# Kernel optimization log

Measured on AMD Instinct MI355X. Metric: run time of the kernel, lower is better.

The kernel has to match this reference:

```python
import jax, jax.numpy as jnp
import numpy as np

B, C, H, W, HEADS = 8, 256, 64, 64, 4
EPS = 1e-5  # torch InstanceNorm2d default eps


def conv1x1(x, w):
    # w: [out_c, in_c]; x: [b, in_c, h, w]
    return jnp.einsum('oc,bchw->bohw', w, x)


def maxpool2(x):
    b, c, h, w = x.shape
    return x.reshape(b, c, h // 2, 2, w // 2, 2).max(axis=(3, 5))


def inorm_affine(x, g, b):
    # InstanceNorm2d(affine=True): normalize per (batch, channel) over H,W
    m = jnp.mean(x, axis=(2, 3), keepdims=True)
    v = jnp.mean((x - m) ** 2, axis=(2, 3), keepdims=True)
    return (x - m) * jax.lax.rsqrt(v + EPS) * g[None, :, None, None] + b[None, :, None, None]


def setup_inputs() -> dict:
    key = jax.random.key(0)
    ks = jax.random.split(key, 12)
    s = 1.0 / np.sqrt(C)  # fan-in style scaling for 1x1 conv weights
    return {
        'x': jax.random.normal(ks[0], (B, C, H, W), jnp.float32),
        'theta_w': jax.random.normal(ks[1], (C, C), jnp.float32) * s,
        'phi_w': jax.random.normal(ks[2], (C, C), jnp.float32) * s,
        'g_w': jax.random.normal(ks[3], (C // 2, C), jnp.float32) * s,
        'o_w': jax.random.normal(ks[4], (C, C // 2), jnp.float32) * np.sqrt(2.0 / C),
        'nt_w': 1.0 + 0.1 * jax.random.normal(ks[5], (C,), jnp.float32),
        'nt_b': 0.1 * jax.random.normal(ks[6], (C,), jnp.float32),
        'np_w': 1.0 + 0.1 * jax.random.normal(ks[7], (C,), jnp.float32),
        'np_b': 0.1 * jax.random.normal(ks[8], (C,), jnp.float32),
        'ng_w': 1.0 + 0.1 * jax.random.normal(ks[9], (C // 2,), jnp.float32),
        'ng_b': 0.1 * jax.random.normal(ks[10], (C // 2,), jnp.float32),
        'gamma': jnp.float32(0.5),
    }


def reference(x, theta_w, phi_w, g_w, o_w, nt_w, nt_b, np_w, np_b, ng_w, ng_b, gamma):
    b, c, h, w = x.shape
    n = h * w            # query length
    m = n // 4           # key/value length after 2x2 maxpool
    theta = inorm_affine(conv1x1(x, theta_w), nt_w, nt_b)
    phi = inorm_affine(maxpool2(conv1x1(x, phi_w)), np_w, np_b)
    g = inorm_affine(maxpool2(conv1x1(x, g_w)), ng_w, ng_b)
    # custom head layout: channel dim split as (C//heads, heads), head dim INNER
    theta_ = theta.reshape(b, c // HEADS, HEADS, n)
    phi_ = phi.reshape(b, c // HEADS, HEADS, m)
    g_ = g.reshape(b, (c // 2) // HEADS, HEADS, m)
    beta = jax.nn.softmax(jnp.einsum('bchi,bchj->bhij', theta_, phi_), axis=-1)
    o = jnp.einsum('bchj,bhij->bchi', g_, beta).reshape(b, c // 2, h, w)
    o = conv1x1(o, o_w)
    return gamma * o + x
```

## Files before the change

### kernel.cpp

```cpp
#include <hip/hip_runtime.h>
#include <hip/hip_bf16.h>
#include <math.h>

typedef float f32x4 __attribute__((ext_vector_type(4)));
typedef float f32x16 __attribute__((ext_vector_type(16)));
typedef __bf16 b16x8 __attribute__((ext_vector_type(8)));
typedef __bf16 b16x4 __attribute__((ext_vector_type(4)));
typedef unsigned int u32x2 __attribute__((ext_vector_type(2)));
typedef unsigned int u32x4 __attribute__((ext_vector_type(4)));

#define L2E 1.44269504088896340736f

__global__ void prep_weights(const float* tw, const float* pw, const float* gw,
                             const float* ow, __bf16* Wp, __bf16* OWp) {
    int idx = blockIdx.x * 256 + threadIdx.x;
    if (idx < 640 * 256) {
        int m = idx >> 8, k = idx & 255;
        float v;
        if (m < 256)      { int o = ((m & 63) << 2) + (m >> 6);            v = tw[o * 256 + k]; }
        else if (m < 512) { int mm = m - 256; int o = ((mm & 63) << 2) + (mm >> 6); v = pw[o * 256 + k]; }
        else              { int mm = m - 512; int o = ((mm & 31) << 2) + (mm >> 5); v = gw[o * 256 + k]; }
        Wp[idx] = (__bf16)v;
    } else {
        int j = idx - 640 * 256;
        if (j < 256 * 128) {
            int m = j >> 7, c = j & 127;
            int o = ((c & 31) << 2) + (c >> 5);
            OWp[j] = (__bf16)ow[m * 128 + o];
        }
    }
}

__global__ __launch_bounds__(256) void conv_gemm(const __bf16* __restrict__ Wp,
                                                 const float* __restrict__ x,
                                                 __bf16* theta_t, __bf16* phi_t, __bf16* g_t) {
    int b = blockIdx.z, mt = blockIdx.y, nt = blockIdx.x;
    __shared__ __bf16 Al[128 * 40];
    __shared__ __bf16 Bl[128 * 40];
    int tid = threadIdx.x, l = tid & 63, w = tid >> 6;
    int wm = w >> 1, wn = w & 1, lr = l & 15, lg = l >> 4;
    f32x4 acc[4][4];
#pragma unroll
    for (int i = 0; i < 4; i++)
#pragma unroll
        for (int j = 0; j < 4; j++)
#pragma unroll
            for (int r = 0; r < 4; r++) acc[i][j][r] = 0.f;
    const __bf16* Ag = Wp + (size_t)mt * 128 * 256;
    const float* Bx = x + (size_t)b * 1048576 + nt * 128;
    int srow = tid >> 2, scol = (tid & 3) * 8;
    int bn = tid & 127, bk0 = (tid >> 7) * 8;
    b16x8 aR[2];
    float xr[2][8];
#pragma unroll
    for (int hh = 0; hh < 2; hh++)
        aR[hh] = *(const b16x8*)&Ag[(size_t)(srow + hh * 64) * 256 + scol];
#pragma unroll
    for (int u = 0; u < 2; u++)
#pragma unroll
        for (int e = 0; e < 8; e++)
            xr[u][e] = Bx[(size_t)(bk0 + u * 16 + e) * 4096 + bn];
    for (int k0 = 0; k0 < 256; k0 += 32) {
        if (k0) __syncthreads();
#pragma unroll
        for (int hh = 0; hh < 2; hh++)
            *(b16x8*)&Al[(srow + hh * 64) * 40 + scol] = aR[hh];
#pragma unroll
        for (int u = 0; u < 2; u++) {
            b16x8 v;
#pragma unroll
            for (int e = 0; e < 8; e++) v[e] = (__bf16)xr[u][e];
            *(b16x8*)&Bl[bn * 40 + bk0 + u * 16] = v;
        }
        __syncthreads();
        if (k0 < 224) {
#pragma unroll
            for (int hh = 0; hh < 2; hh++)
                aR[hh] = *(const b16x8*)&Ag[(size_t)(srow + hh * 64) * 256 + k0 + 32 + scol];
#pragma unroll
            for (int u = 0; u < 2; u++)
#pragma unroll
                for (int e = 0; e < 8; e++)
                    xr[u][e] = Bx[(size_t)(k0 + 32 + bk0 + u * 16 + e) * 4096 + bn];
        }
        int ko = lg * 8;
        b16x8 af[4], bfr[4];
#pragma unroll
        for (int i = 0; i < 4; i++) af[i]  = *(b16x8*)&Al[(wm * 64 + i * 16 + lr) * 40 + ko];
#pragma unroll
        for (int i = 0; i < 4; i++) bfr[i] = *(b16x8*)&Bl[(wn * 64 + i * 16 + lr) * 40 + ko];
#pragma unroll
        for (int i = 0; i < 4; i++)
#pragma unroll
            for (int j = 0; j < 4; j++)
                acc[i][j] = __builtin_amdgcn_mfma_f32_16x16x32_bf16(af[i], bfr[j], acc[i][j], 0, 0, 0);
    }
    int rbase = lg * 4;
#pragma unroll
    for (int i = 0; i < 4; i++) {
        int m = mt * 128 + wm * 64 + i * 16 + rbase;
#pragma unroll
        for (int j = 0; j < 4; j++) {
            int p = nt * 128 + wn * 64 + j * 16 + lr;
            b16x4 v;
#pragma unroll
            for (int r = 0; r < 4; r++) v[r] = (__bf16)acc[i][j][r];
            if (m < 256)      *(b16x4*)&theta_t[((size_t)b * 4096 + p) * 256 + m] = v;
            else if (m < 512) *(b16x4*)&phi_t[((size_t)b * 4096 + p) * 256 + (m - 256)] = v;
            else              *(b16x4*)&g_t[((size_t)b * 4096 + p) * 128 + (m - 512)] = v;
        }
    }
}

__global__ __launch_bounds__(256) void theta_stats(const __bf16* __restrict__ src,
                                                   float* p1, float* p2) {
    __shared__ float S1[8][256], S2[8][256];
    int b = blockIdx.y, blk = blockIdx.x;
    int tid = threadIdx.x, cg = tid & 31, rg = tid >> 5;
    float a1[8], a2[8];
#pragma unroll
    for (int e = 0; e < 8; e++) { a1[e] = 0.f; a2[e] = 0.f; }
    const __bf16* base = src + ((size_t)b * 4096 + blk * 64 + rg * 8) * 256 + cg * 8;
#pragma unroll
    for (int r = 0; r < 8; r++) {
        b16x8 v = *(const b16x8*)&base[(size_t)r * 256];
#pragma unroll
        for (int e = 0; e < 8; e++) { float f = (float)v[e]; a1[e] += f; a2[e] += f * f; }
    }
#pragma unroll
    for (int e = 0; e < 8; e++) { S1[rg][cg * 8 + e] = a1[e]; S2[rg][cg * 8 + e] = a2[e]; }
    __syncthreads();
    float s1 = 0.f, s2 = 0.f;
#pragma unroll
    for (int i = 0; i < 8; i++) { s1 += S1[i][tid]; s2 += S2[i][tid]; }
    p1[(b * 64 + blk) * 256 + tid] = s1;
    p2[(b * 64 + blk) * 256 + tid] = s2;
}

__global__ __launch_bounds__(256) void pool_phi(const __bf16* __restrict__ src, __bf16* dst,
                                                float* p1, float* p2) {
    __shared__ float S1[8][256], S2[8][256];
    int b = blockIdx.y, qc = blockIdx.x;
    int tid = threadIdx.x, cg = tid & 31, qg = tid >> 5;
    float a1[8], a2[8];
#pragma unroll
    for (int e = 0; e < 8; e++) { a1[e] = 0.f; a2[e] = 0.f; }
#pragma unroll
    for (int qq = 0; qq < 4; qq++) {
        int q = qc * 32 + qg * 4 + qq, qy = q >> 5, qx = q & 31;
        size_t base = ((size_t)(b * 4096) + qy * 128 + qx * 2) * 256 + cg * 8;
        b16x8 v0 = *(const b16x8*)&src[base];
        b16x8 v1 = *(const b16x8*)&src[base + 256];
        b16x8 v2 = *(const b16x8*)&src[base + 16384];
        b16x8 v3 = *(const b16x8*)&src[base + 16640];
        b16x8 mv;
#pragma unroll
        for (int e = 0; e < 8; e++) {
            float m = fmaxf(fmaxf((float)v0[e], (float)v1[e]), fmaxf((float)v2[e], (float)v3[e]));
            mv[e] = (__bf16)m; a1[e] += m; a2[e] += m * m;
        }
        *(b16x8*)&dst[((size_t)b * 1024 + q) * 256 + cg * 8] = mv;
    }
#pragma unroll
    for (int e = 0; e < 8; e++) { S1[qg][cg * 8 + e] = a1[e]; S2[qg][cg * 8 + e] = a2[e]; }
    __syncthreads();
    float s1 = 0.f, s2 = 0.f;
#pragma unroll
    for (int i = 0; i < 8; i++) { s1 += S1[i][tid]; s2 += S2[i][tid]; }
    p1[(b * 32 + qc) * 256 + tid] = s1;
    p2[(b * 32 + qc) * 256 + tid] = s2;
}

__global__ __launch_bounds__(256) void pool_gT(const __bf16* __restrict__ src, __bf16* gT,
                                               float* p1, float* p2) {
    __shared__ __bf16 Pt[64][136];
    __shared__ float S1[16][128], S2[16][128];
    int b = blockIdx.y, qc = blockIdx.x;
    int tid = threadIdx.x, cg = tid & 15, qg = tid >> 4;
    float a1[8], a2[8];
#pragma unroll
    for (int e = 0; e < 8; e++) { a1[e] = 0.f; a2[e] = 0.f; }
#pragma unroll
    for (int qq = 0; qq < 4; qq++) {
        int ql = qg * 4 + qq, q = qc * 64 + ql;
        int qy = q >> 5, qx = q & 31;
        size_t base = ((size_t)(b * 4096) + qy * 128 + qx * 2) * 128 + cg * 8;
        b16x8 v0 = *(const b16x8*)&src[base];
        b16x8 v1 = *(const b16x8*)&src[base + 128];
        b16x8 v2 = *(const b16x8*)&src[base + 8192];
        b16x8 v3 = *(const b16x8*)&src[base + 8320];
        b16x8 mv;
#pragma unroll
        for (int e = 0; e < 8; e++) {
            float m = fmaxf(fmaxf((float)v0[e], (float)v1[e]), fmaxf((float)v2[e], (float)v3[e]));
            mv[e] = (__bf16)m; a1[e] += m; a2[e] += m * m;
        }
        *(b16x8*)&Pt[ql][cg * 8] = mv;
    }
#pragma unroll
    for (int e = 0; e < 8; e++) { S1[qg][cg * 8 + e] = a1[e]; S2[qg][cg * 8 + e] = a2[e]; }
    __syncthreads();
    if (tid < 128) {
        float s1 = 0.f, s2 = 0.f;
#pragma unroll
        for (int i = 0; i < 16; i++) { s1 += S1[i][tid]; s2 += S2[i][tid]; }
        p1[(b * 16 + qc) * 128 + tid] = s1;
        p2[(b * 16 + qc) * 128 + tid] = s2;
    }
    int c = tid & 127, qh = tid >> 7;
    int hh = c >> 5, ch = c & 31;
#pragma unroll
    for (int sg = 0; sg < 4; sg++) {
        int seg = qh * 4 + sg;
        b16x8 v;
#pragma unroll
        for (int e = 0; e < 8; e++) v[e] = Pt[seg * 8 + e][c];
        *(b16x8*)&gT[((((size_t)(b * 4 + hh) * 16 + qc) * 8 + seg) * 32 + ch) * 8] = v;
    }
}

__global__ void finalize_stats(const float* tp1, const float* tp2, const float* pp1,
                               const float* pp2, const float* gp1, const float* gp2,
                               const float* ntw, const float* ntb, const float* npw,
                               const float* npb, const float* ngw, const float* ngb,
                               float* sct, float* bit, float* scp, float* bip,
                               float* scg, float* big) {
    int idx = blockIdx.x * 256 + threadIdx.x;
    if (idx >= 8 * 640) return;
    int b = idx / 640, c = idx % 640;
    if (c < 256) {
        float s1 = 0.f, s2 = 0.f;
        for (int i = 0; i < 64; i++) { s1 += tp1[(b * 64 + i) * 256 + c]; s2 += tp2[(b * 64 + i) * 256 + c]; }
        float n = 4096.f;
        float m = s1 / n, v = s2 / n - m * m;
        float r = rsqrtf(v + 1e-5f);
        int o = ((c & 63) << 2) + (c >> 6);
        float wv = ntw[o], bv = ntb[o];
        sct[b * 256 + c] = r * wv * L2E;
        bit[b * 256 + c] = (bv - m * r * wv) * L2E;
    } else if (c < 512) {
        int cc = c - 256;
        float s1 = 0.f, s2 = 0.f;
        for (int i = 0; i < 32; i++) { s1 += pp1[(b * 32 + i) * 256 + cc]; s2 += pp2[(b * 32 + i) * 256 + cc]; }
        float n = 1024.f;
        float m = s1 / n, v = s2 / n - m * m;
        float r = rsqrtf(v + 1e-5f);
        int o = ((cc & 63) << 2) + (cc >> 6);
        float wv = npw[o], bv = npb[o];
        scp[b * 256 + cc] = r * wv; bip[b * 256 + cc] = bv - m * r * wv;
    } else {
        int cc = c - 512;
        float s1 = 0.f, s2 = 0.f;
        for (int i = 0; i < 16; i++) { s1 += gp1[(b * 16 + i) * 128 + cc]; s2 += gp2[(b * 16 + i) * 128 + cc]; }
        float n = 1024.f;
        float m = s1 / n, v = s2 / n - m * m;
        float r = rsqrtf(v + 1e-5f);
        int o = ((cc & 31) << 2) + (cc >> 5);
        float wv = ngw[o], bv = ngb[o];
        scg[b * 128 + cc] = r * wv; big[b * 128 + cc] = bv - m * r * wv;
    }
}

__global__ void normalize_phi(const __bf16* __restrict__ php, __bf16* __restrict__ phk,
                              const float* __restrict__ scp, const float* __restrict__ bip) {
    int blk = blockIdx.x, t = threadIdx.x;
    int b = blk >> 6, h = (blk >> 4) & 3, cc = blk & 15;
#pragma unroll
    for (int uu = 0; uu < 2; uu++) {
        int u = uu * 256 + t;
        int slot = u >> 6, key = u & 63;
        int q = cc * 64 + key;
        int cfull = h * 64 + (slot >> 1) * 16 + (slot & 1) * 8;
        b16x8 v = *(const b16x8*)&php[((size_t)b * 1024 + q) * 256 + cfull];
        b16x8 nv;
#pragma unroll
        for (int e = 0; e < 8; e++)
            nv[e] = (__bf16)((float)v[e] * scp[b * 256 + cfull + e] + bip[b * 256 + cfull + e]);
        *(b16x8*)&phk[((((size_t)(b * 4 + h) * 16 + cc) * 8 + slot) * 64 + key) * 8] = nv;
    }
}

__global__ __launch_bounds__(256, 2) void attn(const __bf16* __restrict__ theta_t,
                                               const __bf16* __restrict__ phk,
                                               const __bf16* __restrict__ gTz,
                                               const float* __restrict__ sct,
                                               const float* __restrict__ bit,
                                               const float* __restrict__ scg,
                                               const float* __restrict__ big,
                                               __bf16* __restrict__ o_mid) {
    __shared__ __bf16 Kb[3][4096];
    __shared__ __bf16 Vb[3][2048];
    int bid = blockIdx.x;
    int idx = bid >> 3;
    int bh = (bid & 7) * 4 + (idx >> 5), qt = idx & 31;
    int b = bh >> 2, h = bh & 3;
    int tid = threadIdx.x, w = tid >> 6, lane = tid & 63;
    int l31 = lane & 31, hi = lane >> 5;
    int q = qt * 128 + w * 32 + l31;

    b16x8 qf[4];
    {
        const __bf16* qp = theta_t + ((size_t)b * 4096 + q) * 256 + h * 64;
#pragma unroll
        for (int st = 0; st < 4; st++) {
            int cb = st * 16 + hi * 8;
            b16x8 raw = *(const b16x8*)&qp[cb];
            b16x8 nv;
#pragma unroll
            for (int e = 0; e < 8; e++) {
                int cix = b * 256 + h * 64 + cb + e;
                nv[e] = (__bf16)((float)raw[e] * sct[cix] + bit[cix]);
            }
            qf[st] = nv;
        }
    }

    const __bf16* Kg = phk + (size_t)bh * 65536;
    const __bf16* Vg = gTz + (size_t)bh * 32768;

    f32x16 oacc;
    float l_run = 0.f;
#pragma unroll
    for (int r = 0; r < 16; r++) oacc[r] = 0.f;
    f32x16 zc;
#pragma unroll
    for (int r = 0; r < 16; r++) zc[r] = 0.f;

#define ISSUE(buf, cc) { \
    __builtin_amdgcn_global_load_lds( \
        (const __attribute__((address_space(1))) void*)(Kg + (size_t)(cc) * 4096 + (w * 2) * 512 + lane * 8), \
        (__attribute__((address_space(3))) void*)(&Kb[buf][(w * 2) * 512]), 16, 0, 0); \
    __builtin_amdgcn_global_load_lds( \
        (const __attribute__((address_space(1))) void*)(Kg + (size_t)(cc) * 4096 + (w * 2 + 1) * 512 + lane * 8), \
        (__attribute__((address_space(3))) void*)(&Kb[buf][(w * 2 + 1) * 512]), 16, 0, 0); \
    __builtin_amdgcn_global_load_lds( \
        (const __attribute__((address_space(1))) void*)(Vg + (size_t)(cc) * 2048 + w * 512 + lane * 8), \
        (__attribute__((address_space(3))) void*)(&Vb[buf][w * 512]), 16, 0, 0); }

#define COMPUTE(cur) { \
    b16x8 ak[2][4], av[4]; \
    _Pragma("unroll") for (int kf = 0; kf < 2; kf++) \
    _Pragma("unroll") for (int st = 0; st < 4; st++) \
        ak[kf][st] = *(b16x8*)&Kb[cur][(st * 2 + hi) * 512 + (kf * 32 + l31) * 8]; \
    _Pragma("unroll") for (int js = 0; js < 4; js++) \
        av[js] = *(b16x8*)&Vb[cur][((js * 2 + hi) * 32 + l31) * 8]; \
    _Pragma("unroll") for (int kf = 0; kf < 2; kf++) { \
        f32x16 s = __builtin_amdgcn_mfma_f32_32x32x16_bf16(ak[kf][0], qf[0], zc, 0, 0, 0); \
        _Pragma("unroll") for (int st = 1; st < 4; st++) \
            s = __builtin_amdgcn_mfma_f32_32x32x16_bf16(ak[kf][st], qf[st], s, 0, 0, 0); \
        float s0 = 0.f, s1 = 0.f, s2p = 0.f, s3 = 0.f; \
        _Pragma("unroll") for (int r = 0; r < 16; r += 4) { \
            float p0 = __builtin_amdgcn_exp2f(s[r]); \
            float p1 = __builtin_amdgcn_exp2f(s[r + 1]); \
            float p2 = __builtin_amdgcn_exp2f(s[r + 2]); \
            float p3 = __builtin_amdgcn_exp2f(s[r + 3]); \
            s[r] = p0; s[r + 1] = p1; s[r + 2] = p2; s[r + 3] = p3; \
            s0 += p0; s1 += p1; s2p += p2; s3 += p3; \
        } \
        l_run += (s0 + s1) + (s2p + s3); \
        _Pragma("unroll") for (int hh2 = 0; hh2 < 2; hh2++) { \
            b16x4 A4, B4; \
            _Pragma("unroll") for (int e = 0; e < 4; e++) { \
                A4[e] = (__bf16)s[hh2 * 8 + e]; B4[e] = (__bf16)s[hh2 * 8 + 4 + e]; } \
            u32x2 a2 = __builtin_bit_cast(u32x2, A4); \
            u32x2 b2 = __builtin_bit_cast(u32x2, B4); \
            u32x2 q0 = __builtin_amdgcn_permlane32_swap(a2[0], b2[0], false, false); \
            u32x2 q1 = __builtin_amdgcn_permlane32_swap(a2[1], b2[1], false, false); \
            u32x4 pd = {q0[0], q1[0], q0[1], q1[1]}; \
            b16x8 pf = __builtin_bit_cast(b16x8, pd); \
            oacc = __builtin_amdgcn_mfma_f32_32x32x16_bf16(av[kf * 2 + hh2], pf, oacc, 0, 0, 0); \
        } \
    } }

    ISSUE(0, 0)
    ISSUE(1, 1)
#pragma unroll 1
    for (int c = 0; c < 16; c++) {
        if (c < 15) { asm volatile("s_waitcnt vmcnt(3)" ::: "memory"); }
        else        { asm volatile("s_waitcnt vmcnt(0)" ::: "memory"); }
        __builtin_amdgcn_s_barrier();
        __builtin_amdgcn_sched_barrier(0);
        if (c + 2 < 16) { int ib = (c + 2) % 3; ISSUE(ib, c + 2) }
        COMPUTE(c % 3)
    }
#undef ISSUE
#undef COMPUTE

    {
        float lr = l_run + __shfl_xor(l_run, 32, 64);
        float rl = 1.0f / lr;
#pragma unroll
        for (int rr = 0; rr < 4; rr++) {
            b16x4 v;
#pragma unroll
            for (int e = 0; e < 4; e++) {
                int ci = b * 128 + h * 32 + rr * 8 + hi * 4 + e;
                v[e] = (__bf16)(oacc[rr * 4 + e] * rl * scg[ci] + big[ci]);
            }
            *(b16x4*)&o_mid[((size_t)b * 4096 + q) * 128 + h * 32 + rr * 8 + hi * 4] = v;
        }
    }
}

__global__ __launch_bounds__(256) void out_gemm(const __bf16* __restrict__ OWp,
                                                const __bf16* __restrict__ o_mid,
                                                const float* __restrict__ x,
                                                const float* gamma, float* out) {
    int b = blockIdx.z, mt = blockIdx.y, nt = blockIdx.x;
    __shared__ __bf16 Al[128 * 40];
    __shared__ __bf16 Bl[128 * 40];
    int tid = threadIdx.x, l = tid & 63, w = tid >> 6;
    int wm = w >> 1, wn = w & 1, lr = l & 15, lg = l >> 4;
    f32x4 acc[4][4];
#pragma unroll
    for (int i = 0; i < 4; i++)
#pragma unroll
        for (int j = 0; j < 4; j++)
#pragma unroll
            for (int r = 0; r < 4; r++) acc[i][j][r] = 0.f;
    const __bf16* Ag = OWp + (size_t)mt * 128 * 128;
    const __bf16* Bg = o_mid + ((size_t)b * 4096 + nt * 128) * 128;
    int srow = tid >> 2, scol = (tid & 3) * 8;
    b16x8 aR[2], bR[2];
#pragma unroll
    for (int hh = 0; hh < 2; hh++) {
        int r = srow + hh * 64;
        aR[hh] = *(const b16x8*)&Ag[(size_t)r * 128 + scol];
        bR[hh] = *(const b16x8*)&Bg[(size_t)r * 128 + scol];
    }
    for (int k0 = 0; k0 < 128; k0 += 32) {
        if (k0) __syncthreads();
#pragma unroll
        for (int hh = 0; hh < 2; hh++) {
            int r = srow + hh * 64;
            *(b16x8*)&Al[r * 40 + scol] = aR[hh];
            *(b16x8*)&Bl[r * 40 + scol] = bR[hh];
        }
        __syncthreads();
        if (k0 < 96) {
#pragma unroll
            for (int hh = 0; hh < 2; hh++) {
                int r = srow + hh * 64;
                aR[hh] = *(const b16x8*)&Ag[(size_t)r * 128 + k0 + 32 + scol];
                bR[hh] = *(const b16x8*)&Bg[(size_t)r * 128 + k0 + 32 + scol];
            }
        }
        int ko = lg * 8;
        b16x8 af[4], bfr[4];
#pragma unroll
        for (int i = 0; i < 4; i++) af[i]  = *(b16x8*)&Al[(wm * 64 + i * 16 + lr) * 40 + ko];
#pragma unroll
        for (int i = 0; i < 4; i++) bfr[i] = *(b16x8*)&Bl[(wn * 64 + i * 16 + lr) * 40 + ko];
#pragma unroll
        for (int i = 0; i < 4; i++)
#pragma unroll
            for (int j = 0; j < 4; j++)
                acc[i][j] = __builtin_amdgcn_mfma_f32_16x16x32_bf16(af[i], bfr[j], acc[i][j], 0, 0, 0);
    }
    float gm = gamma[0];
    int rbase = lg * 4;
#pragma unroll
    for (int i = 0; i < 4; i++) {
        int m = mt * 128 + wm * 64 + i * 16 + rbase;
#pragma unroll
        for (int j = 0; j < 4; j++) {
            int p = nt * 128 + wn * 64 + j * 16 + lr;
#pragma unroll
            for (int r = 0; r < 4; r++) {
                size_t o = ((size_t)b * 256 + m + r) * 4096 + p;
                out[o] = gm * acc[i][j][r] + x[o];
            }
        }
    }
}

extern "C" void kernel_launch(void* const* d_in, const int* in_sizes, int n_in,
                              void* d_out, int out_size, void* d_ws, size_t ws_size,
                              hipStream_t stream) {
    const float* x   = (const float*)d_in[0];
    const float* tw  = (const float*)d_in[1];
    const float* pw  = (const float*)d_in[2];
    const float* gw  = (const float*)d_in[3];
    const float* ow  = (const float*)d_in[4];
    const float* ntw = (const float*)d_in[5];
    const float* ntb = (const float*)d_in[6];
    const float* npw = (const float*)d_in[7];
    const float* npb = (const float*)d_in[8];
    const float* ngw = (const float*)d_in[9];
    const float* ngb = (const float*)d_in[10];
    const float* gamma = (const float*)d_in[11];
    float* out = (float*)d_out;
    char* ws = (char*)d_ws;

    __bf16* Wp  = (__bf16*)(ws + 0);
    __bf16* OWp = (__bf16*)(ws + 327680);
    __bf16* th  = (__bf16*)(ws + 17170432);
    __bf16* phr = (__bf16*)(ws + 33947648);
    __bf16* ghr = (__bf16*)(ws + 50724864);
    __bf16* php = (__bf16*)(ws + 59113472);
    __bf16* gT  = (__bf16*)(ws + 63307776);
    float* sb   = (float*)(ws + 65445888);

    float* tp1 = (float*)(ws + 393216);
    float* tp2 = (float*)(ws + 917504);
    float* pp1 = (float*)(ws + 1441792);
    float* pp2 = (float*)(ws + 1703936);
    float* gp1 = (float*)(ws + 1966080);
    float* gp2 = (float*)(ws + 2031616);
    __bf16* phk = phr;
    __bf16* om  = (__bf16*)(ws + 2097152);

    float *sct = sb, *bit = sb + 2048, *scp = sb + 4096, *bip = sb + 6144,
          *scg = sb + 8192, *big = sb + 9216;

    prep_weights<<<768, 256, 0, stream>>>(tw, pw, gw, ow, Wp, OWp);
    conv_gemm<<<dim3(32, 5, 8), 256, 0, stream>>>(Wp, x, th, phr, ghr);
    theta_stats<<<dim3(64, 8), 256, 0, stream>>>(th, tp1, tp2);
    pool_phi<<<dim3(32, 8), 256, 0, stream>>>(phr, php, pp1, pp2);
    pool_gT<<<dim3(16, 8), 256, 0, stream>>>(ghr, gT, gp1, gp2);
    finalize_stats<<<20, 256, 0, stream>>>(tp1, tp2, pp1, pp2, gp1, gp2,
                                           ntw, ntb, npw, npb, ngw, ngb,
                                           sct, bit, scp, bip, scg, big);
    normalize_phi<<<512, 256, 0, stream>>>(php, phk, scp, bip);
    attn<<<1024, 256, 0, stream>>>(th, phk, gT, sct, bit, scg, big, om);
    out_gemm<<<dim3(32, 2, 8), 256, 0, stream>>>(OWp, om, x, gamma, out);
}
```

Before: 120.2 us.

## Fuse theta stats into conv GEMM, register-prefetch attention K/V, nontemporal output

Theta per-channel sum and sum-of-squares are now reduced inside the conv GEMM epilogue with lane shuffles, which removes the separate theta_stats kernel and its re-read of theta. The attention kernel drops its LDS triple buffering and barriers in favour of per-lane global loads into registers, prefetching the next K/V chunk while the current one is computed. The output GEMM writes with nontemporal stores. Register-prefetched attention raises register pressure and relies on global-load latency being hidden without LDS sharing. The stats now come from fp32 accumulators rather than bf16-rounded values.

```diff
diff --git a/kernel.cpp b/kernel.cpp
--- a/kernel.cpp
+++ b/kernel.cpp
@@ -33,7 +33,8 @@
 
 __global__ __launch_bounds__(256) void conv_gemm(const __bf16* __restrict__ Wp,
                                                  const float* __restrict__ x,
-                                                 __bf16* theta_t, __bf16* phi_t, __bf16* g_t) {
+                                                 __bf16* theta_t, __bf16* phi_t, __bf16* g_t,
+                                                 float* tp1, float* tp2) {
     int b = blockIdx.z, mt = blockIdx.y, nt = blockIdx.x;
     __shared__ __bf16 Al[128 * 40];
     __shared__ __bf16 Bl[128 * 40];
@@ -95,6 +96,34 @@
             for (int j = 0; j < 4; j++)
                 acc[i][j] = __builtin_amdgcn_mfma_f32_16x16x32_bf16(af[i], bfr[j], acc[i][j], 0, 0, 0);
     }
+    if (mt < 2) {
+#pragma unroll
+        for (int i = 0; i < 4; i++) {
+            float s1v[4], s2v[4];
+#pragma unroll
+            for (int r = 0; r < 4; r++) {
+                float a0 = acc[i][0][r], a1 = acc[i][1][r], a2 = acc[i][2][r], a3 = acc[i][3][r];
+                s1v[r] = (a0 + a1) + (a2 + a3);
+                s2v[r] = (a0 * a0 + a1 * a1) + (a2 * a2 + a3 * a3);
+            }
+#pragma unroll
+            for (int msk = 1; msk < 16; msk <<= 1)
+#pragma unroll
+                for (int r = 0; r < 4; r++) {
+                    s1v[r] += __shfl_xor(s1v[r], msk, 64);
+                    s2v[r] += __shfl_xor(s2v[r], msk, 64);
+                }
+            if (lr == 0) {
+                int row = (b * 32 + nt) * 2 + wn;
+#pragma unroll
+                for (int r = 0; r < 4; r++) {
+                    int ch = mt * 128 + wm * 64 + i * 16 + lg * 4 + r;
+                    tp1[row * 256 + ch] = s1v[r];
+                    tp2[row * 256 + ch] = s2v[r];
+                }
+            }
+        }
+    }
     int rbase = lg * 4;
 #pragma unroll
     for (int i = 0; i < 4; i++) {
@@ -110,31 +139,6 @@
             else              *(b16x4*)&g_t[((size_t)b * 4096 + p) * 128 + (m - 512)] = v;
         }
     }
-}
-
-__global__ __launch_bounds__(256) void theta_stats(const __bf16* __restrict__ src,
-                                                   float* p1, float* p2) {
-    __shared__ float S1[8][256], S2[8][256];
-    int b = blockIdx.y, blk = blockIdx.x;
-    int tid = threadIdx.x, cg = tid & 31, rg = tid >> 5;
-    float a1[8], a2[8];
-#pragma unroll
-    for (int e = 0; e < 8; e++) { a1[e] = 0.f; a2[e] = 0.f; }
-    const __bf16* base = src + ((size_t)b * 4096 + blk * 64 + rg * 8) * 256 + cg * 8;
-#pragma unroll
-    for (int r = 0; r < 8; r++) {
-        b16x8 v = *(const b16x8*)&base[(size_t)r * 256];
-#pragma unroll
-        for (int e = 0; e < 8; e++) { float f = (float)v[e]; a1[e] += f; a2[e] += f * f; }
-    }
-#pragma unroll
-    for (int e = 0; e < 8; e++) { S1[rg][cg * 8 + e] = a1[e]; S2[rg][cg * 8 + e] = a2[e]; }
-    __syncthreads();
-    float s1 = 0.f, s2 = 0.f;
-#pragma unroll
-    for (int i = 0; i < 8; i++) { s1 += S1[i][tid]; s2 += S2[i][tid]; }
-    p1[(b * 64 + blk) * 256 + tid] = s1;
-    p2[(b * 64 + blk) * 256 + tid] = s2;
 }
 
 __global__ __launch_bounds__(256) void pool_phi(const __bf16* __restrict__ src, __bf16* dst,
@@ -280,16 +284,14 @@
     }
 }
 
-__global__ __launch_bounds__(256, 2) void attn(const __bf16* __restrict__ theta_t,
-                                               const __bf16* __restrict__ phk,
-                                               const __bf16* __restrict__ gTz,
-                                               const float* __restrict__ sct,
-                                               const float* __restrict__ bit,
-                                               const float* __restrict__ scg,
-                                               const float* __restrict__ big,
-                                               __bf16* __restrict__ o_mid) {
-    __shared__ __bf16 Kb[3][4096];
-    __shared__ __bf16 Vb[3][2048];
+__global__ __launch_bounds__(256) void attn(const __bf16* __restrict__ theta_t,
+                                            const __bf16* __restrict__ phk,
+                                            const __bf16* __restrict__ gTz,
+                                            const float* __restrict__ sct,
+                                            const float* __restrict__ bit,
+                                            const float* __restrict__ scg,
+                                            const float* __restrict__ big,
+                                            __bf16* __restrict__ o_mid) {
     int bid = blockIdx.x;
     int idx = bid >> 3;
     int bh = (bid & 7) * 4 + (idx >> 5), qt = idx & 31;
@@ -315,8 +317,8 @@
         }
     }
 
-    const __bf16* Kg = phk + (size_t)bh * 65536;
-    const __bf16* Vg = gTz + (size_t)bh * 32768;
+    const __bf16* Kg = phk + (size_t)bh * 65536 + hi * 512 + l31 * 8;
+    const __bf16* Vg = gTz + (size_t)bh * 32768 + hi * 256 + l31 * 8;
 
     f32x16 oacc;
     float l_run = 0.f;
@@ -326,65 +328,65 @@
 #pragma unroll
     for (int r = 0; r < 16; r++) zc[r] = 0.f;
 
-#define ISSUE(buf, cc) { \
-    __builtin_amdgcn_global_load_lds( \
-        (const __attribute__((address_space(1))) void*)(Kg + (size_t)(cc) * 4096 + (w * 2) * 512 + lane * 8), \
-        (__attribute__((address_space(3))) void*)(&Kb[buf][(w * 2) * 512]), 16, 0, 0); \
-    __builtin_amdgcn_global_load_lds( \
-        (const __attribute__((address_space(1))) void*)(Kg + (size_t)(cc) * 4096 + (w * 2 + 1) * 512 + lane * 8), \
-        (__attribute__((address_space(3))) void*)(&Kb[buf][(w * 2 + 1) * 512]), 16, 0, 0); \
-    __builtin_amdgcn_global_load_lds( \
-        (const __attribute__((address_space(1))) void*)(Vg + (size_t)(cc) * 2048 + w * 512 + lane * 8), \
-        (__attribute__((address_space(3))) void*)(&Vb[buf][w * 512]), 16, 0, 0); }
-
-#define COMPUTE(cur) { \
-    b16x8 ak[2][4], av[4]; \
-    _Pragma("unroll") for (int kf = 0; kf < 2; kf++) \
+    b16x8 ak[2][4], av[4], avn[4];
+
+#define LOADK(dst, c) { _Pragma("unroll") for (int kf = 0; kf < 2; kf++) \
     _Pragma("unroll") for (int st = 0; st < 4; st++) \
-        ak[kf][st] = *(b16x8*)&Kb[cur][(st * 2 + hi) * 512 + (kf * 32 + l31) * 8]; \
-    _Pragma("unroll") for (int js = 0; js < 4; js++) \
-        av[js] = *(b16x8*)&Vb[cur][((js * 2 + hi) * 32 + l31) * 8]; \
-    _Pragma("unroll") for (int kf = 0; kf < 2; kf++) { \
-        f32x16 s = __builtin_amdgcn_mfma_f32_32x32x16_bf16(ak[kf][0], qf[0], zc, 0, 0, 0); \
-        _Pragma("unroll") for (int st = 1; st < 4; st++) \
-            s = __builtin_amdgcn_mfma_f32_32x32x16_bf16(ak[kf][st], qf[st], s, 0, 0, 0); \
-        float s0 = 0.f, s1 = 0.f, s2p = 0.f, s3 = 0.f; \
-        _Pragma("unroll") for (int r = 0; r < 16; r += 4) { \
-            float p0 = __builtin_amdgcn_exp2f(s[r]); \
-            float p1 = __builtin_amdgcn_exp2f(s[r + 1]); \
-            float p2 = __builtin_amdgcn_exp2f(s[r + 2]); \
-            float p3 = __builtin_amdgcn_exp2f(s[r + 3]); \
-            s[r] = p0; s[r + 1] = p1; s[r + 2] = p2; s[r + 3] = p3; \
-            s0 += p0; s1 += p1; s2p += p2; s3 += p3; \
-        } \
-        l_run += (s0 + s1) + (s2p + s3); \
-        _Pragma("unroll") for (int hh2 = 0; hh2 < 2; hh2++) { \
-            b16x4 A4, B4; \
-            _Pragma("unroll") for (int e = 0; e < 4; e++) { \
-                A4[e] = (__bf16)s[hh2 * 8 + e]; B4[e] = (__bf16)s[hh2 * 8 + 4 + e]; } \
-            u32x2 a2 = __builtin_bit_cast(u32x2, A4); \
-            u32x2 b2 = __builtin_bit_cast(u32x2, B4); \
-            u32x2 q0 = __builtin_amdgcn_permlane32_swap(a2[0], b2[0], false, false); \
-            u32x2 q1 = __builtin_amdgcn_permlane32_swap(a2[1], b2[1], false, false); \
-            u32x4 pd = {q0[0], q1[0], q0[1], q1[1]}; \
-            b16x8 pf = __builtin_bit_cast(b16x8, pd); \
-            oacc = __builtin_amdgcn_mfma_f32_32x32x16_bf16(av[kf * 2 + hh2], pf, oacc, 0, 0, 0); \
-        } \
-    } }
-
-    ISSUE(0, 0)
-    ISSUE(1, 1)
+        dst[kf][st] = *(const b16x8*)&Kg[(size_t)(c) * 4096 + st * 1024 + kf * 256]; }
+#define LOADV(dst, c) { _Pragma("unroll") for (int js = 0; js < 4; js++) \
+    dst[js] = *(const b16x8*)&Vg[(size_t)(c) * 2048 + js * 512]; }
+
+    LOADK(ak, 0) LOADV(av, 0)
 #pragma unroll 1
-    for (int c = 0; c < 16; c++) {
-        if (c < 15) { asm volatile("s_waitcnt vmcnt(3)" ::: "memory"); }
-        else        { asm volatile("s_waitcnt vmcnt(0)" ::: "memory"); }
-        __builtin_amdgcn_s_barrier();
-        __builtin_amdgcn_sched_barrier(0);
-        if (c + 2 < 16) { int ib = (c + 2) % 3; ISSUE(ib, c + 2) }
-        COMPUTE(c % 3)
-    }
-#undef ISSUE
-#undef COMPUTE
+    for (int c = 0; c < 16; ++c) {
+        f32x16 s[2];
+#pragma unroll
+        for (int kf = 0; kf < 2; kf++) {
+            s[kf] = __builtin_amdgcn_mfma_f32_32x32x16_bf16(ak[kf][0], qf[0], zc, 0, 0, 0);
+#pragma unroll
+            for (int st = 1; st < 4; st++)
+                s[kf] = __builtin_amdgcn_mfma_f32_32x32x16_bf16(ak[kf][st], qf[st], s[kf], 0, 0, 0);
+        }
+        if (c < 15) { LOADK(ak, c + 1) }
+        float s0 = 0.f, s1 = 0.f, s2p = 0.f, s3 = 0.f;
+#pragma unroll
+        for (int kf = 0; kf < 2; kf++)
+#pragma unroll
+            for (int r = 0; r < 16; r += 4) {
+                float p0 = __builtin_amdgcn_exp2f(s[kf][r]);
+                float p1 = __builtin_amdgcn_exp2f(s[kf][r + 1]);
+                float p2 = __builtin_amdgcn_exp2f(s[kf][r + 2]);
+                float p3 = __builtin_amdgcn_exp2f(s[kf][r + 3]);
+                s[kf][r] = p0; s[kf][r + 1] = p1; s[kf][r + 2] = p2; s[kf][r + 3] = p3;
+                s0 += p0; s1 += p1; s2p += p2; s3 += p3;
+            }
+        l_run += (s0 + s1) + (s2p + s3);
+        if (c < 15) { LOADV(avn, c + 1) }
+#pragma unroll
+        for (int kf = 0; kf < 2; kf++)
+#pragma unroll
+            for (int hh2 = 0; hh2 < 2; hh2++) {
+                b16x4 A4, B4;
+#pragma unroll
+                for (int e = 0; e < 4; e++) {
+                    A4[e] = (__bf16)s[kf][hh2 * 8 + e];
+                    B4[e] = (__bf16)s[kf][hh2 * 8 + 4 + e];
+                }
+                u32x2 a2 = __builtin_bit_cast(u32x2, A4);
+                u32x2 b2 = __builtin_bit_cast(u32x2, B4);
+                u32x2 q0 = __builtin_amdgcn_permlane32_swap(a2[0], b2[0], false, false);
+                u32x2 q1 = __builtin_amdgcn_permlane32_swap(a2[1], b2[1], false, false);
+                u32x4 pd = {q0[0], q1[0], q0[1], q1[1]};
+                b16x8 pf = __builtin_bit_cast(b16x8, pd);
+                oacc = __builtin_amdgcn_mfma_f32_32x32x16_bf16(av[kf * 2 + hh2], pf, oacc, 0, 0, 0);
+            }
+        if (c < 15) {
+#pragma unroll
+            for (int js = 0; js < 4; js++) av[js] = avn[js];
+        }
+    }
+#undef LOADK
+#undef LOADV
 
     {
         float lr = l_run + __shfl_xor(l_run, 32, 64);
@@ -468,7 +470,7 @@
 #pragma unroll
             for (int r = 0; r < 4; r++) {
                 size_t o = ((size_t)b * 256 + m + r) * 4096 + p;
-                out[o] = gm * acc[i][j][r] + x[o];
+                __builtin_nontemporal_store(gm * acc[i][j][r] + x[o], &out[o]);
             }
         }
     }
@@ -514,8 +516,7 @@
           *scg = sb + 8192, *big = sb + 9216;
 
     prep_weights<<<768, 256, 0, stream>>>(tw, pw, gw, ow, Wp, OWp);
-    conv_gemm<<<dim3(32, 5, 8), 256, 0, stream>>>(Wp, x, th, phr, ghr);
-    theta_stats<<<dim3(64, 8), 256, 0, stream>>>(th, tp1, tp2);
+    conv_gemm<<<dim3(32, 5, 8), 256, 0, stream>>>(Wp, x, th, phr, ghr, tp1, tp2);
     pool_phi<<<dim3(32, 8), 256, 0, stream>>>(phr, php, pp1, pp2);
     pool_gT<<<dim3(16, 8), 256, 0, stream>>>(ghr, gT, gp1, gp2);
     finalize_stats<<<20, 256, 0, stream>>>(tp1, tp2, pp1, pp2, gp1, gp2,
```

Measured after the change: 124.4 us. 1.03x slower.
